# Performance work log

Hardware: AMD Instinct MI355X
Metric: run time of the kernel (lower is better)

The kernel has to match this reference:

```python
import jax, jax.numpy as jnp
import numpy as np

NUM_SEGMENTS = 2048
EPS = 1e-6

def setup_inputs() -> dict:
    key = jax.random.key(0)
    k1, k2 = jax.random.split(key)
    N, D = 1000000, 64
    x = jax.random.normal(k1, (N, D), dtype=jnp.float32)
    seg = jnp.sort(jax.random.randint(k2, (N,), 0, NUM_SEGMENTS, dtype=jnp.int32))
    return {"x": x, "seg": seg}

def reference(x, seg):
    # Per-segment SCALAR min/max over all nodes and features of each graph,
    # matching torch's x.min()/x.max() on each unbatched segment.
    row_min = jnp.min(x, axis=1)  # [N]
    row_max = jnp.max(x, axis=1)  # [N]
    g_min = jax.ops.segment_min(row_min, seg, num_segments=NUM_SEGMENTS)  # [G]
    g_max = jax.ops.segment_max(row_max, seg, num_segments=NUM_SEGMENTS)  # [G]
    mn = g_min[seg][:, None]  # [N,1]
    mx = g_max[seg][:, None]  # [N,1]
    return (x - mn) / (mx - mn + EPS)
```

## Files before the change

kernel.cpp:

```cpp
#include <hip/hip_runtime.h>

#define NSEG 2048
#define EPS 1e-6f
#define BLK 1024
#define RPT 10

typedef float nfloat4 __attribute__((ext_vector_type(4)));

__global__ void starts_k(const int* __restrict__ seg, int* __restrict__ starts, int n) {
    int i = blockIdx.x * blockDim.x + threadIdx.x;
    if (i >= n) return;
    int s = seg[i];
    int prev = (i == 0) ? -1 : seg[i - 1];
    for (int k = prev + 1; k <= s; ++k) starts[k] = i;
    if (i == n - 1) {
        for (int k = s + 1; k <= NSEG; ++k) starts[k] = n;
    }
}

__device__ __forceinline__ void wave_reduce(float& mn, float& mx) {
#pragma unroll
    for (int off = 32; off; off >>= 1) {
        mn = fminf(mn, __shfl_xor(mn, off));
        mx = fmaxf(mx, __shfl_xor(mx, off));
    }
}

__device__ __forceinline__ void min4max4(const float4& v, float& mn, float& mx) {
    mn = fminf(mn, fminf(fminf(v.x, v.y), fminf(v.z, v.w)));
    mx = fmaxf(mx, fmaxf(fmaxf(v.x, v.y), fmaxf(v.z, v.w)));
}

__global__ __launch_bounds__(BLK, 4) void norm_seg(const float4* __restrict__ x4,
                                                   const int* __restrict__ starts,
                                                   nfloat4* __restrict__ out4) {
    const int b = blockIdx.x;
    const long f0 = (long)starts[b] * 16;
    const int n = (int)((long)starts[b + 1] * 16 - f0);
    if (n <= 0) return;
    const int t = threadIdx.x;
    __shared__ float2 red[BLK / 64];

    float lmin = INFINITY, lmax = -INFINITY;

    if (n <= BLK * RPT) {
        float4 v[RPT];
#pragma unroll
        for (int i = 0; i < RPT; ++i) {
            int idx = i * BLK + t;
            if (idx < n) v[i] = x4[f0 + idx];
        }
#pragma unroll
        for (int i = 0; i < RPT; ++i) {
            int idx = i * BLK + t;
            if (idx < n) min4max4(v[i], lmin, lmax);
        }
        wave_reduce(lmin, lmax);
        if ((t & 63) == 0) red[t >> 6] = make_float2(lmin, lmax);
        __syncthreads();
        float mn = INFINITY, mx = -INFINITY;
#pragma unroll
        for (int w = 0; w < BLK / 64; ++w) {
            mn = fminf(mn, red[w].x);
            mx = fmaxf(mx, red[w].y);
        }
        const float sc = 1.0f / (mx - mn + EPS);
#pragma unroll
        for (int i = 0; i < RPT; ++i) {
            int idx = i * BLK + t;
            if (idx < n) {
                nfloat4 o;
                o.x = (v[i].x - mn) * sc;
                o.y = (v[i].y - mn) * sc;
                o.z = (v[i].z - mn) * sc;
                o.w = (v[i].w - mn) * sc;
                __builtin_nontemporal_store(o, &out4[f0 + idx]);
            }
        }
    } else {
        for (int base = 0; base < n; base += BLK * RPT) {
            float4 v[RPT];
#pragma unroll
            for (int i = 0; i < RPT; ++i) {
                int idx = base + i * BLK + t;
                if (idx < n) v[i] = x4[f0 + idx];
            }
#pragma unroll
            for (int i = 0; i < RPT; ++i) {
                int idx = base + i * BLK + t;
                if (idx < n) min4max4(v[i], lmin, lmax);
            }
        }
        wave_reduce(lmin, lmax);
        if ((t & 63) == 0) red[t >> 6] = make_float2(lmin, lmax);
        __syncthreads();
        float mn = INFINITY, mx = -INFINITY;
#pragma unroll
        for (int w = 0; w < BLK / 64; ++w) {
            mn = fminf(mn, red[w].x);
            mx = fmaxf(mx, red[w].y);
        }
        const float sc = 1.0f / (mx - mn + EPS);
        for (int base = 0; base < n; base += BLK * RPT) {
#pragma unroll
            for (int i = 0; i < RPT; ++i) {
                int idx = base + i * BLK + t;
                if (idx < n) {
                    float4 v = x4[f0 + idx];
                    nfloat4 o;
                    o.x = (v.x - mn) * sc;
                    o.y = (v.y - mn) * sc;
                    o.z = (v.z - mn) * sc;
                    o.w = (v.w - mn) * sc;
                    __builtin_nontemporal_store(o, &out4[f0 + idx]);
                }
            }
        }
    }
}

extern "C" void kernel_launch(void* const* d_in, const int* in_sizes, int n_in,
                              void* d_out, int out_size, void* d_ws, size_t ws_size,
                              hipStream_t stream) {
    const float4* x4 = (const float4*)d_in[0];
    const int* seg = (const int*)d_in[1];
    nfloat4* out4 = (nfloat4*)d_out;
    const int nrows = in_sizes[1];

    int* starts = (int*)d_ws;

    starts_k<<<(nrows + 255) / 256, 256, 0, stream>>>(seg, starts, nrows);
    norm_seg<<<NSEG, BLK, 0, stream>>>(x4, starts, out4);
}
```

Measured before the change: 431.1 us.

## Process eight segments per block with double-buffered register prefetch

Each block now handles 8 consecutive segments instead of one, so the grid shrinks to 256 blocks. While segment k is being reduced and written, the loads for segment k+1 are issued into a second register buffer, overlapping loads with the reduction and stores. The fallback path for oversized segments is rewritten to loop per segment with one float4 per thread per step. With only 256 blocks of 1024 threads on a GPU with 256 CUs, the risk is lower occupancy and less memory-level parallelism, plus the register pressure of twenty float4 values per thread.

```diff
diff --git a/kernel.cpp b/kernel.cpp
--- a/kernel.cpp
+++ b/kernel.cpp
@@ -4,6 +4,8 @@
 #define EPS 1e-6f
 #define BLK 1024
 #define RPT 10
+#define SPB 8
+#define GRID (NSEG / SPB)
 
 typedef float nfloat4 __attribute__((ext_vector_type(4)));
 
@@ -34,87 +36,112 @@
 __global__ __launch_bounds__(BLK, 4) void norm_seg(const float4* __restrict__ x4,
                                                    const int* __restrict__ starts,
                                                    nfloat4* __restrict__ out4) {
-    const int b = blockIdx.x;
-    const long f0 = (long)starts[b] * 16;
-    const int n = (int)((long)starts[b + 1] * 16 - f0);
-    if (n <= 0) return;
     const int t = threadIdx.x;
-    __shared__ float2 red[BLK / 64];
+    __shared__ float2 red[2][BLK / 64];
 
-    float lmin = INFINITY, lmax = -INFINITY;
+    int st[SPB + 1];
+#pragma unroll
+    for (int j = 0; j <= SPB; ++j) st[j] = starts[blockIdx.x * SPB + j];
 
-    if (n <= BLK * RPT) {
-        float4 v[RPT];
+    bool big = false;
 #pragma unroll
-        for (int i = 0; i < RPT; ++i) {
-            int idx = i * BLK + t;
-            if (idx < n) v[i] = x4[f0 + idx];
+    for (int j = 0; j < SPB; ++j) big |= (st[j + 1] - st[j]) > BLK * RPT / 16;
+
+    if (!big) {
+        float4 vb[2][RPT];
+
+        {
+            const long f0 = (long)st[0] * 16;
+            const int n0 = (st[1] - st[0]) * 16;
+#pragma unroll
+            for (int i = 0; i < RPT; ++i) {
+                int idx = i * BLK + t;
+                if (idx < n0) vb[0][i] = x4[f0 + idx];
+            }
         }
+
 #pragma unroll
-        for (int i = 0; i < RPT; ++i) {
-            int idx = i * BLK + t;
-            if (idx < n) min4max4(v[i], lmin, lmax);
-        }
-        wave_reduce(lmin, lmax);
-        if ((t & 63) == 0) red[t >> 6] = make_float2(lmin, lmax);
-        __syncthreads();
-        float mn = INFINITY, mx = -INFINITY;
+        for (int k = 0; k < SPB; ++k) {
+            const int cur = k & 1, nxt = cur ^ 1;
+            const long fk = (long)st[k] * 16;
+            const int nk = (st[k + 1] - st[k]) * 16;
+
+            float lmin = INFINITY, lmax = -INFINITY;
 #pragma unroll
-        for (int w = 0; w < BLK / 64; ++w) {
-            mn = fminf(mn, red[w].x);
-            mx = fmaxf(mx, red[w].y);
-        }
-        const float sc = 1.0f / (mx - mn + EPS);
+            for (int i = 0; i < RPT; ++i) {
+                int idx = i * BLK + t;
+                if (idx < nk) min4max4(vb[cur][i], lmin, lmax);
+            }
+            wave_reduce(lmin, lmax);
+            if ((t & 63) == 0) red[cur][t >> 6] = make_float2(lmin, lmax);
+            __syncthreads();
+            float mn = INFINITY, mx = -INFINITY;
 #pragma unroll
-        for (int i = 0; i < RPT; ++i) {
-            int idx = i * BLK + t;
-            if (idx < n) {
-                nfloat4 o;
-                o.x = (v[i].x - mn) * sc;
-                o.y = (v[i].y - mn) * sc;
-                o.z = (v[i].z - mn) * sc;
-                o.w = (v[i].w - mn) * sc;
-                __builtin_nontemporal_store(o, &out4[f0 + idx]);
+            for (int w = 0; w < BLK / 64; ++w) {
+                mn = fminf(mn, red[cur][w].x);
+                mx = fmaxf(mx, red[cur][w].y);
+            }
+            const float sc = 1.0f / (mx - mn + EPS);
+
+            if (k + 1 < SPB) {
+                const long fn = (long)st[k + 1] * 16;
+                const int nn = (st[k + 2] - st[k + 1]) * 16;
+#pragma unroll
+                for (int i = 0; i < RPT; ++i) {
+                    int idx = i * BLK + t;
+                    if (idx < nn) vb[nxt][i] = x4[fn + idx];
+                }
+            }
+
+#pragma unroll
+            for (int i = 0; i < RPT; ++i) {
+                int idx = i * BLK + t;
+                if (idx < nk) {
+                    nfloat4 o;
+                    o.x = (vb[cur][i].x - mn) * sc;
+                    o.y = (vb[cur][i].y - mn) * sc;
+                    o.z = (vb[cur][i].z - mn) * sc;
+                    o.w = (vb[cur][i].w - mn) * sc;
+                    __builtin_nontemporal_store(o, &out4[fk + idx]);
+                }
             }
         }
     } else {
-        for (int base = 0; base < n; base += BLK * RPT) {
-            float4 v[RPT];
+        for (int k = 0; k < SPB; ++k) {
+            const long fk = (long)st[k] * 16;
+            const int nk = (st[k + 1] - st[k]) * 16;
+            if (nk <= 0) { __syncthreads(); __syncthreads(); continue; }
+            float lmin = INFINITY, lmax = -INFINITY;
+            for (int base = 0; base < nk; base += BLK) {
+                int idx = base + t;
+                if (idx < nk) {
+                    float4 v = x4[fk + idx];
+                    min4max4(v, lmin, lmax);
+                }
+            }
+            wave_reduce(lmin, lmax);
+            if ((t & 63) == 0) red[0][t >> 6] = make_float2(lmin, lmax);
+            __syncthreads();
+            float mn = INFINITY, mx = -INFINITY;
 #pragma unroll
-            for (int i = 0; i < RPT; ++i) {
-                int idx = base + i * BLK + t;
-                if (idx < n) v[i] = x4[f0 + idx];
+            for (int w = 0; w < BLK / 64; ++w) {
+                mn = fminf(mn, red[0][w].x);
+                mx = fmaxf(mx, red[0][w].y);
             }
-#pragma unroll
-            for (int i = 0; i < RPT; ++i) {
-                int idx = base + i * BLK + t;
-                if (idx < n) min4max4(v[i], lmin, lmax);
-            }
-        }
-        wave_reduce(lmin, lmax);
-        if ((t & 63) == 0) red[t >> 6] = make_float2(lmin, lmax);
-        __syncthreads();
-        float mn = INFINITY, mx = -INFINITY;
-#pragma unroll
-        for (int w = 0; w < BLK / 64; ++w) {
-            mn = fminf(mn, red[w].x);
-            mx = fmaxf(mx, red[w].y);
-        }
-        const float sc = 1.0f / (mx - mn + EPS);
-        for (int base = 0; base < n; base += BLK * RPT) {
-#pragma unroll
-            for (int i = 0; i < RPT; ++i) {
-                int idx = base + i * BLK + t;
-                if (idx < n) {
-                    float4 v = x4[f0 + idx];
+            const float sc = 1.0f / (mx - mn + EPS);
+            for (int base = 0; base < nk; base += BLK) {
+                int idx = base + t;
+                if (idx < nk) {
+                    float4 v = x4[fk + idx];
                     nfloat4 o;
                     o.x = (v.x - mn) * sc;
                     o.y = (v.y - mn) * sc;
                     o.z = (v.z - mn) * sc;
                     o.w = (v.w - mn) * sc;
-                    __builtin_nontemporal_store(o, &out4[f0 + idx]);
+                    __builtin_nontemporal_store(o, &out4[fk + idx]);
                 }
             }
+            __syncthreads();
         }
     }
 }
@@ -130,5 +157,5 @@
     int* starts = (int*)d_ws;
 
     starts_k<<<(nrows + 255) / 256, 256, 0, stream>>>(seg, starts, nrows);
-    norm_seg<<<NSEG, BLK, 0, stream>>>(x4, starts, out4);
+    norm_seg<<<GRID, BLK, 0, stream>>>(x4, starts, out4);
 }
```

New measurement: 444.0 us. +3.0%, slower.
